# Optimization experiments

Hardware: AMD Instinct MI355X
Metric: run time of the kernel (lower is better)

## Reference

```python
import jax, jax.numpy as jnp
import numpy as np

EPS = 0.1        # SinkhornDistance eps (hard-coded in SGE.__init__)
MAX_ITER = 10    # SinkhornDistance max_iter
THRESH = 0.1     # early-exit threshold in SinkhornDistance.forward
N_POINTS = 32
SPACE_DIM = 16   # emb_dim // n_points = 512 // 32


def _sinkhorn_cost(x, y):
    """Regularized OT cost between point clouds x, y: [B, P, D] -> [B]."""
    # C[b,i,j] = sum_d |x[b,i,d] - y[b,j,d]|^2
    C = jnp.sum(jnp.square(jnp.abs(x[:, :, None, :] - y[:, None, :, :])), axis=-1)
    B, P1 = x.shape[0], x.shape[1]
    P2 = y.shape[1]
    mu = jnp.full((B, P1), 1.0 / P1, dtype=x.dtype)
    nu = jnp.full((B, P2), 1.0 / P2, dtype=x.dtype)

    def M(u, v):
        # (-C + u_i + v_j) / eps
        return (-C + u[:, :, None] + v[:, None, :]) / EPS

    def step(carry, _):
        u, v, done = carry
        u_new = EPS * (jnp.log(mu + 1e-8) - jax.nn.logsumexp(M(u, v), axis=-1)) + u
        v_new = EPS * (jnp.log(nu + 1e-8)
                       - jax.nn.logsumexp(M(u_new, v).swapaxes(-2, -1), axis=-1)) + v
        err = jnp.mean(jnp.sum(jnp.abs(u_new - u), axis=-1))
        u2 = jnp.where(done, u, u_new)
        v2 = jnp.where(done, v, v_new)
        done2 = done | (err < THRESH)  # torch breaks AFTER applying the update
        return (u2, v2, done2), None

    init = (jnp.zeros_like(mu), jnp.zeros_like(nu), jnp.array(False))
    (u, v, _), _ = jax.lax.scan(step, init, None, length=MAX_ITER)
    pi = jnp.exp(M(u, v))
    return jnp.sum(pi * C, axis=(-2, -1))  # [B]


def setup_inputs() -> dict:
    key = jax.random.key(0)
    k1, k2, k3, k4 = jax.random.split(key, 4)
    n_nodes, feat, emb, n_edges = 10000, 256, 512, 4096
    x = jax.random.normal(k1, (n_nodes, feat), dtype=jnp.float32)
    W = jax.random.normal(k2, (feat, emb), dtype=jnp.float32) / np.float32(np.sqrt(feat))
    edges_pos = jax.random.randint(k3, (2, n_edges), 0, n_nodes)
    edges_neg = jax.random.randint(k4, (2, n_edges), 0, n_nodes)
    return {"x": x, "W": W, "edges_pos": edges_pos, "edges_neg": edges_neg}


def reference(x, W, edges_pos, edges_neg):
    z = x @ W  # encoder: linear projection [n_nodes, emb_dim]

    def score_pairs(nx, ny):
        a = z[nx].reshape(-1, N_POINTS, SPACE_DIM)
        b = z[ny].reshape(-1, N_POINTS, SPACE_DIM)
        return -_sinkhorn_cost(a, b)

    pos_energy = score_pairs(edges_pos[0], edges_pos[1])
    neg_energy = score_pairs(edges_neg[0], edges_neg[1])
    loss = jnp.mean(pos_energy ** 2 + jnp.exp(neg_energy))
    return loss
```

## Files before the change

kernel.cpp:

```cpp
#include <hip/hip_runtime.h>
#include <hip/hip_bf16.h>
#include <math.h>

#define N_POINTS 32
#define SPACE_DIM 16
#define EMB 512
#define THRESH 0.1f
#define MAX_ITER 10
#define KDIM 256

#define NEG10LOG2E -14.42695040888963f
#define EPS_LN2     0.0693147180559945f
#define LOGMU2     -4.99999953834f

typedef _Float16 half8 __attribute__((ext_vector_type(8)));
typedef _Float16 half4 __attribute__((ext_vector_type(4)));
typedef float floatx4 __attribute__((ext_vector_type(4)));

#define BSTRIDE 264

__global__ __launch_bounds__(256) void gemm_fused(
    const float* __restrict__ X, const float* __restrict__ W,
    float* __restrict__ Z, int M, int K, int N)
{
    (void)K;

    __shared__ _Float16 Bs[64][BSTRIDE];

    int t = threadIdx.x;
    int n0 = blockIdx.y * 64;

    int wave = t >> 6;
    int lane = t & 63;
    int quad = lane >> 4;
    int l16 = lane & 15;

    int mrow = blockIdx.x * 64 + wave * 16 + l16;
    int msafe = mrow < M ? mrow : M - 1;
    const float4* xp = (const float4*)(X + (size_t)msafe * KDIM);

    float4 xr[16];
    #pragma unroll
    for (int kk = 0; kk < 8; ++kk) {
        xr[2 * kk]     = xp[kk * 8 + quad * 2];
        xr[2 * kk + 1] = xp[kk * 8 + quad * 2 + 1];
    }

    #pragma unroll
    for (int s = 0; s < 4; ++s) {
        int u = s * 256 + t;
        int nb = u & 15;
        int kb = u >> 4;
        float4 r0v = *(const float4*)&W[(size_t)(kb * 4 + 0) * N + n0 + nb * 4];
        float4 r1v = *(const float4*)&W[(size_t)(kb * 4 + 1) * N + n0 + nb * 4];
        float4 r2v = *(const float4*)&W[(size_t)(kb * 4 + 2) * N + n0 + nb * 4];
        float4 r3v = *(const float4*)&W[(size_t)(kb * 4 + 3) * N + n0 + nb * 4];
        float c0[4] = {r0v.x, r0v.y, r0v.z, r0v.w};
        float c1[4] = {r1v.x, r1v.y, r1v.z, r1v.w};
        float c2[4] = {r2v.x, r2v.y, r2v.z, r2v.w};
        float c3[4] = {r3v.x, r3v.y, r3v.z, r3v.w};
        #pragma unroll
        for (int c = 0; c < 4; ++c) {
            half4 h = {(_Float16)c0[c], (_Float16)c1[c],
                       (_Float16)c2[c], (_Float16)c3[c]};
            *(half4*)&Bs[nb * 4 + c][kb * 4] = h;
        }
    }
    __syncthreads();

    floatx4 acc[4] = {{0.f,0.f,0.f,0.f},{0.f,0.f,0.f,0.f},
                      {0.f,0.f,0.f,0.f},{0.f,0.f,0.f,0.f}};

    #pragma unroll
    for (int kk = 0; kk < 8; ++kk) {
        float4 lo = xr[2 * kk];
        float4 hi = xr[2 * kk + 1];
        half8 a = {(_Float16)lo.x, (_Float16)lo.y, (_Float16)lo.z, (_Float16)lo.w,
                   (_Float16)hi.x, (_Float16)hi.y, (_Float16)hi.z, (_Float16)hi.w};
        #pragma unroll
        for (int ct = 0; ct < 4; ++ct) {
            half8 b = *(const half8*)&Bs[ct * 16 + l16][kk * 32 + quad * 8];
            acc[ct] = __builtin_amdgcn_mfma_f32_16x16x32_f16(a, b, acc[ct], 0, 0, 0);
        }
    }

    int rbase = blockIdx.x * 64 + wave * 16 + quad * 4;
    #pragma unroll
    for (int ct = 0; ct < 4; ++ct) {
        int col = n0 + ct * 16 + l16;
        #pragma unroll
        for (int r = 0; r < 4; ++r) {
            int row = rbase + r;
            if (row < M) Z[(size_t)row * N + col] = acc[ct][r];
        }
    }
}

#define WPB 4

__global__ __launch_bounds__(256, 4) void sinkhorn_fused(
    const float* __restrict__ Z,
    const int* __restrict__ ep, const int* __restrict__ en,
    int nE,
    float* __restrict__ cost_all,
    float* __restrict__ err_part)
{
    __shared__ float shm[WPB][32 * 36];
    __shared__ float uvs[WPB][64];

    int tid = threadIdx.x;
    int wv = tid >> 6;
    int t = tid & 63;
    int b = blockIdx.x * WPB + wv;

    int side = (b >= nE) ? 1 : 0;
    int e = b - side * nE;
    const int* edges = side ? en : ep;
    int nx = edges[e];
    int ny = edges[e + nE];

    int c = t & 31;
    int h = t >> 5;
    int r0 = h * 16;

    float* sb  = shm[wv];
    float* csh = shm[wv];
    float* Ul  = uvs[wv];
    float* Vl  = uvs[wv] + 32;

    {
        const float4* zb4 = (const float4*)(Z + (size_t)ny * EMB);
        float4 q0 = zb4[t * 2];
        float4 q1 = zb4[t * 2 + 1];
        float* dst = sb + (t >> 1) * 20 + (t & 1) * 8;
        ((float4*)dst)[0] = q0;
        ((float4*)dst)[1] = q1;
    }
    float areg[16];
    {
        const float4* za4 = (const float4*)(Z + (size_t)nx * EMB + c * SPACE_DIM);
        float4 a0 = za4[0], a1 = za4[1], a2 = za4[2], a3 = za4[3];
        areg[0]=a0.x; areg[1]=a0.y; areg[2]=a0.z; areg[3]=a0.w;
        areg[4]=a1.x; areg[5]=a1.y; areg[6]=a1.z; areg[7]=a1.w;
        areg[8]=a2.x; areg[9]=a2.y; areg[10]=a2.z; areg[11]=a2.w;
        areg[12]=a3.x; areg[13]=a3.y; areg[14]=a3.z; areg[15]=a3.w;
    }

    float Crow[16];
    #pragma unroll
    for (int jj = 0; jj < 16; ++jj) {
        const float* bp = sb + (r0 + jj) * 20;
        float s = 0.f;
        #pragma unroll
        for (int d = 0; d < SPACE_DIM; ++d) {
            float diff = areg[d] - bp[d];
            s = fmaf(diff, diff, s);
        }
        Crow[jj] = s * NEG10LOG2E;
    }
    #pragma unroll
    for (int g = 0; g < 4; ++g) {
        *(float4*)&csh[c * 36 + r0 + g * 4] =
            make_float4(Crow[g*4+0], Crow[g*4+1], Crow[g*4+2], Crow[g*4+3]);
    }
    float Ccol[16];
    #pragma unroll
    for (int ii = 0; ii < 16; ++ii)
        Ccol[ii] = csh[(r0 + ii) * 36 + c];

    Vl[c] = 0.f;
    float U = 0.f;
    float ccp[MAX_ITER];
    float dup[MAX_ITER];

    #pragma unroll
    for (int it = 0; it < MAX_ITER; ++it) {
        float w[16];
        {
            const float4* vp = (const float4*)(Vl + r0);
            float4 v0 = vp[0], v1 = vp[1], v2 = vp[2], v3 = vp[3];
            float vv[16] = {v0.x,v0.y,v0.z,v0.w, v1.x,v1.y,v1.z,v1.w,
                            v2.x,v2.y,v2.z,v2.w, v3.x,v3.y,v3.z,v3.w};
            #pragma unroll
            for (int jj = 0; jj < 16; ++jj) w[jj] = Crow[jj] + vv[jj];
        }
        float m8[8];
        #pragma unroll
        for (int k = 0; k < 8; ++k) m8[k] = fmaxf(w[k], w[k + 8]);
        float m4a = fmaxf(m8[0], m8[4]), m4b = fmaxf(m8[1], m8[5]);
        float m4c = fmaxf(m8[2], m8[6]), m4d = fmaxf(m8[3], m8[7]);
        float mx = fmaxf(fmaxf(m4a, m4b), fmaxf(m4c, m4d));
        mx = fmaxf(mx, __shfl_xor(mx, 32));

        float ex[16];
        #pragma unroll
        for (int jj = 0; jj < 16; ++jj) ex[jj] = __builtin_amdgcn_exp2f(w[jj] - mx);
        float s8[8], p8[8];
        #pragma unroll
        for (int k = 0; k < 8; ++k) {
            s8[k] = ex[k] + ex[k + 8];
            p8[k] = fmaf(ex[k], Crow[k], ex[k + 8] * Crow[k + 8]);
        }
        float sm = ((s8[0]+s8[4]) + (s8[1]+s8[5])) + ((s8[2]+s8[6]) + (s8[3]+s8[7]));
        float pc = ((p8[0]+p8[4]) + (p8[1]+p8[5])) + ((p8[2]+p8[6]) + (p8[3]+p8[7]));
        sm += __shfl_xor(sm, 32);

        if (it > 0) ccp[it - 1] = __builtin_amdgcn_exp2f(U + mx) * pc;

        float Un = LOGMU2 - (mx + __builtin_amdgcn_logf(sm));
        dup[it] = fabsf(Un - U);
        U = Un;
        Ul[c] = U;

        float wc[16];
        {
            const float4* up = (const float4*)(Ul + r0);
            float4 u0 = up[0], u1 = up[1], u2 = up[2], u3 = up[3];
            float uu[16] = {u0.x,u0.y,u0.z,u0.w, u1.x,u1.y,u1.z,u1.w,
                            u2.x,u2.y,u2.z,u2.w, u3.x,u3.y,u3.z,u3.w};
            #pragma unroll
            for (int ii = 0; ii < 16; ++ii) wc[ii] = Ccol[ii] + uu[ii];
        }
        float n8[8];
        #pragma unroll
        for (int k = 0; k < 8; ++k) n8[k] = fmaxf(wc[k], wc[k + 8]);
        float n4a = fmaxf(n8[0], n8[4]), n4b = fmaxf(n8[1], n8[5]);
        float n4c = fmaxf(n8[2], n8[6]), n4d = fmaxf(n8[3], n8[7]);
        float mx2 = fmaxf(fmaxf(n4a, n4b), fmaxf(n4c, n4d));
        mx2 = fmaxf(mx2, __shfl_xor(mx2, 32));

        float e2[16];
        #pragma unroll
        for (int ii = 0; ii < 16; ++ii) e2[ii] = __builtin_amdgcn_exp2f(wc[ii] - mx2);
        float t8[8];
        #pragma unroll
        for (int k = 0; k < 8; ++k) t8[k] = e2[k] + e2[k + 8];
        float sm2 = ((t8[0]+t8[4]) + (t8[1]+t8[5])) + ((t8[2]+t8[6]) + (t8[3]+t8[7]));
        sm2 += __shfl_xor(sm2, 32);
        float Vn = LOGMU2 - (mx2 + __builtin_amdgcn_logf(sm2));
        Vl[c] = Vn;
    }

    {
        const float4* vp = (const float4*)(Vl + r0);
        float4 v0 = vp[0], v1 = vp[1], v2 = vp[2], v3 = vp[3];
        float vv[16] = {v0.x,v0.y,v0.z,v0.w, v1.x,v1.y,v1.z,v1.w,
                        v2.x,v2.y,v2.z,v2.w, v3.x,v3.y,v3.z,v3.w};
        float cc = 0.f;
        #pragma unroll
        for (int jj = 0; jj < 16; ++jj)
            cc = fmaf(__builtin_amdgcn_exp2f(U + Crow[jj] + vv[jj]), Crow[jj], cc);
        ccp[MAX_ITER - 1] = cc;
    }

    #pragma unroll
    for (int m = 1; m < 32; m <<= 1) {
        #pragma unroll
        for (int k = 0; k < MAX_ITER; ++k) {
            dup[k] += __shfl_xor(dup[k], m);
            ccp[k] += __shfl_xor(ccp[k], m);
        }
    }
    #pragma unroll
    for (int k = 0; k < MAX_ITER; ++k) ccp[k] += __shfl_xor(ccp[k], 32);

    if (t == 0) {
        #pragma unroll
        for (int k = 0; k < MAX_ITER; ++k)
            cost_all[(size_t)k * (2 * nE) + b] = -EPS_LN2 * ccp[k];
        #pragma unroll
        for (int k = 0; k < MAX_ITER; ++k) uvs[wv][k] = dup[k];
    }
    __syncthreads();

    if (tid < MAX_ITER) {
        float s4 = uvs[0][tid] + uvs[1][tid] + uvs[2][tid] + uvs[3][tid];
        err_part[(size_t)tid * gridDim.x + blockIdx.x] = EPS_LN2 * s4;
    }
}

__global__ __launch_bounds__(256) void finalize(
    const float* __restrict__ err_part,
    const float* __restrict__ cost_all,
    float* __restrict__ out, int nE, int nB)
{
    __shared__ float em_s[2 * MAX_ITER];
    __shared__ float red[4];

    int tid = threadIdx.x;
    int wv = tid >> 6;
    int t = tid & 63;

    for (int r = wv; r < MAX_ITER; r += 4) {
        const float4* p4 = (const float4*)(err_part + (size_t)r * nB);
        float4 v0 = p4[t       ], v1 = p4[t +  64], v2 = p4[t + 128], v3 = p4[t + 192];
        float4 v4 = p4[t + 256], v5 = p4[t + 320], v6 = p4[t + 384], v7 = p4[t + 448];
        float ps = ((v0.x+v0.y)+(v0.z+v0.w)) + ((v1.x+v1.y)+(v1.z+v1.w))
                 + ((v2.x+v2.y)+(v2.z+v2.w)) + ((v3.x+v3.y)+(v3.z+v3.w));
        float ns = ((v4.x+v4.y)+(v4.z+v4.w)) + ((v5.x+v5.y)+(v5.z+v5.w))
                 + ((v6.x+v6.y)+(v6.z+v6.w)) + ((v7.x+v7.y)+(v7.z+v7.w));
        #pragma unroll
        for (int m = 1; m < 64; m <<= 1) {
            ps += __shfl_xor(ps, m);
            ns += __shfl_xor(ns, m);
        }
        if (t == 0) {
            em_s[r] = ps / (float)nE;
            em_s[MAX_ITER + r] = ns / (float)nE;
        }
    }
    __syncthreads();

    int Tp = MAX_ITER, Tn = MAX_ITER;
    for (int i = 0; i < MAX_ITER; ++i)
        if (em_s[i] < THRESH) { Tp = i + 1; break; }
    for (int i = 0; i < MAX_ITER; ++i)
        if (em_s[MAX_ITER + i] < THRESH) { Tn = i + 1; break; }

    const float4* cp4 = (const float4*)(cost_all + (size_t)(Tp - 1) * (2 * nE));
    const float4* cn4 = (const float4*)(cost_all + (size_t)(Tn - 1) * (2 * nE) + nE);
    float4 p0 = cp4[tid      ], p1 = cp4[tid + 256],
           p2 = cp4[tid + 512], p3 = cp4[tid + 768];
    float4 n0 = cn4[tid      ], n1 = cn4[tid + 256],
           n2 = cn4[tid + 512], n3 = cn4[tid + 768];
    float aP = 0.f;
    aP = fmaf(p0.x,p0.x,aP); aP = fmaf(p0.y,p0.y,aP);
    aP = fmaf(p0.z,p0.z,aP); aP = fmaf(p0.w,p0.w,aP);
    aP = fmaf(p1.x,p1.x,aP); aP = fmaf(p1.y,p1.y,aP);
    aP = fmaf(p1.z,p1.z,aP); aP = fmaf(p1.w,p1.w,aP);
    aP = fmaf(p2.x,p2.x,aP); aP = fmaf(p2.y,p2.y,aP);
    aP = fmaf(p2.z,p2.z,aP); aP = fmaf(p2.w,p2.w,aP);
    aP = fmaf(p3.x,p3.x,aP); aP = fmaf(p3.y,p3.y,aP);
    aP = fmaf(p3.z,p3.z,aP); aP = fmaf(p3.w,p3.w,aP);
    float aN = 0.f;
    aN += expf(-n0.x) + expf(-n0.y) + expf(-n0.z) + expf(-n0.w);
    aN += expf(-n1.x) + expf(-n1.y) + expf(-n1.z) + expf(-n1.w);
    aN += expf(-n2.x) + expf(-n2.y) + expf(-n2.z) + expf(-n2.w);
    aN += expf(-n3.x) + expf(-n3.y) + expf(-n3.z) + expf(-n3.w);
    float acc = aP + aN;
    #pragma unroll
    for (int m = 1; m < 64; m <<= 1) acc += __shfl_xor(acc, m);
    if (t == 0) red[wv] = acc;
    __syncthreads();
    if (tid == 0)
        out[0] = ((red[0] + red[1]) + (red[2] + red[3])) / (float)nE;
}

extern "C" void kernel_launch(void* const* d_in, const int* in_sizes, int n_in,
                              void* d_out, int out_size, void* d_ws, size_t ws_size,
                              hipStream_t stream)
{
    const float* X = (const float*)d_in[0];
    const float* W = (const float*)d_in[1];
    const int* ep = (const int*)d_in[2];
    const int* en = (const int*)d_in[3];
    float* out = (float*)d_out;

    int K = in_sizes[1] / EMB;
    int M = in_sizes[0] / K;
    int nE = in_sizes[2] / 2;

    float* ws = (float*)d_ws;
    float* Z = ws;
    float* cost_all = Z + (size_t)M * EMB;
    float* err_part = cost_all + (size_t)MAX_ITER * 2 * nE;

    dim3 gg((M + 63) / 64, EMB / 64);
    gemm_fused<<<gg, 256, 0, stream>>>(X, W, Z, M, K, EMB);

    int nblk = (2 * nE) / WPB;
    sinkhorn_fused<<<nblk, 64 * WPB, 0, stream>>>(Z, ep, en, nE,
                                                  cost_all, err_part);

    finalize<<<1, 256, 0, stream>>>(err_part, cost_all, out, nE, nblk);
}
```

Baseline: 136.5 us.

## Widen GEMM blocks to 256 columns with double-buffered W staging

Each GEMM block now covers 256 output columns in four 64-column chunks instead of one, so the X rows are loaded and converted to fp16 once and reused across the chunks. The W tile for the next chunk is staged into a second shared-memory buffer while the current chunk runs its MFMAs, overlapping global loads with compute. The grid shrinks from 8 to 2 column blocks, which cuts redundant X traffic but lowers parallelism (about 314 blocks) and doubles LDS use per block, which can reduce occupancy.

```diff
diff --git a/kernel.cpp b/kernel.cpp
--- a/kernel.cpp
+++ b/kernel.cpp
@@ -25,73 +25,81 @@
 {
     (void)K;
 
-    __shared__ _Float16 Bs[64][BSTRIDE];
+    __shared__ _Float16 Bs[2][64][BSTRIDE];
 
     int t = threadIdx.x;
-    int n0 = blockIdx.y * 64;
-
     int wave = t >> 6;
     int lane = t & 63;
     int quad = lane >> 4;
     int l16 = lane & 15;
+    int n_base = blockIdx.y * 256;
 
     int mrow = blockIdx.x * 64 + wave * 16 + l16;
     int msafe = mrow < M ? mrow : M - 1;
     const float4* xp = (const float4*)(X + (size_t)msafe * KDIM);
 
-    float4 xr[16];
+    half8 ah[8];
     #pragma unroll
     for (int kk = 0; kk < 8; ++kk) {
-        xr[2 * kk]     = xp[kk * 8 + quad * 2];
-        xr[2 * kk + 1] = xp[kk * 8 + quad * 2 + 1];
-    }
-
-    #pragma unroll
-    for (int s = 0; s < 4; ++s) {
-        int u = s * 256 + t;
-        int nb = u & 15;
-        int kb = u >> 4;
-        float4 r0v = *(const float4*)&W[(size_t)(kb * 4 + 0) * N + n0 + nb * 4];
-        float4 r1v = *(const float4*)&W[(size_t)(kb * 4 + 1) * N + n0 + nb * 4];
-        float4 r2v = *(const float4*)&W[(size_t)(kb * 4 + 2) * N + n0 + nb * 4];
-        float4 r3v = *(const float4*)&W[(size_t)(kb * 4 + 3) * N + n0 + nb * 4];
-        float c0[4] = {r0v.x, r0v.y, r0v.z, r0v.w};
-        float c1[4] = {r1v.x, r1v.y, r1v.z, r1v.w};
-        float c2[4] = {r2v.x, r2v.y, r2v.z, r2v.w};
-        float c3[4] = {r3v.x, r3v.y, r3v.z, r3v.w};
-        #pragma unroll
-        for (int c = 0; c < 4; ++c) {
-            half4 h = {(_Float16)c0[c], (_Float16)c1[c],
-                       (_Float16)c2[c], (_Float16)c3[c]};
-            *(half4*)&Bs[nb * 4 + c][kb * 4] = h;
-        }
-    }
-    __syncthreads();
-
-    floatx4 acc[4] = {{0.f,0.f,0.f,0.f},{0.f,0.f,0.f,0.f},
-                      {0.f,0.f,0.f,0.f},{0.f,0.f,0.f,0.f}};
-
-    #pragma unroll
-    for (int kk = 0; kk < 8; ++kk) {
-        float4 lo = xr[2 * kk];
-        float4 hi = xr[2 * kk + 1];
-        half8 a = {(_Float16)lo.x, (_Float16)lo.y, (_Float16)lo.z, (_Float16)lo.w,
-                   (_Float16)hi.x, (_Float16)hi.y, (_Float16)hi.z, (_Float16)hi.w};
+        float4 lo = xp[kk * 8 + quad * 2];
+        float4 hi = xp[kk * 8 + quad * 2 + 1];
+        ah[kk] = (half8){(_Float16)lo.x, (_Float16)lo.y, (_Float16)lo.z, (_Float16)lo.w,
+                         (_Float16)hi.x, (_Float16)hi.y, (_Float16)hi.z, (_Float16)hi.w};
+    }
+
+    auto stage = [&](int buf, int ct2) {
+        int n0 = n_base + ct2 * 64;
+        #pragma unroll
+        for (int s = 0; s < 4; ++s) {
+            int u = s * 256 + t;
+            int nb = u & 15;
+            int kb = u >> 4;
+            float4 r0v = *(const float4*)&W[(size_t)(kb * 4 + 0) * N + n0 + nb * 4];
+            float4 r1v = *(const float4*)&W[(size_t)(kb * 4 + 1) * N + n0 + nb * 4];
+            float4 r2v = *(const float4*)&W[(size_t)(kb * 4 + 2) * N + n0 + nb * 4];
+            float4 r3v = *(const float4*)&W[(size_t)(kb * 4 + 3) * N + n0 + nb * 4];
+            float c0[4] = {r0v.x, r0v.y, r0v.z, r0v.w};
+            float c1[4] = {r1v.x, r1v.y, r1v.z, r1v.w};
+            float c2[4] = {r2v.x, r2v.y, r2v.z, r2v.w};
+            float c3[4] = {r3v.x, r3v.y, r3v.z, r3v.w};
+            #pragma unroll
+            for (int c = 0; c < 4; ++c) {
+                half4 h = {(_Float16)c0[c], (_Float16)c1[c],
+                           (_Float16)c2[c], (_Float16)c3[c]};
+                *(half4*)&Bs[buf][nb * 4 + c][kb * 4] = h;
+            }
+        }
+    };
+
+    stage(0, 0);
+
+    int rbase = blockIdx.x * 64 + wave * 16 + quad * 4;
+
+    #pragma unroll
+    for (int ct2 = 0; ct2 < 4; ++ct2) {
+        __syncthreads();
+        if (ct2 < 3) stage((ct2 + 1) & 1, ct2 + 1);
+
+        int cur = ct2 & 1;
+        floatx4 acc[4] = {{0.f,0.f,0.f,0.f},{0.f,0.f,0.f,0.f},
+                          {0.f,0.f,0.f,0.f},{0.f,0.f,0.f,0.f}};
+        #pragma unroll
+        for (int kk = 0; kk < 8; ++kk) {
+            #pragma unroll
+            for (int ct = 0; ct < 4; ++ct) {
+                half8 b = *(const half8*)&Bs[cur][ct * 16 + l16][kk * 32 + quad * 8];
+                acc[ct] = __builtin_amdgcn_mfma_f32_16x16x32_f16(ah[kk], b, acc[ct], 0, 0, 0);
+            }
+        }
+
         #pragma unroll
         for (int ct = 0; ct < 4; ++ct) {
-            half8 b = *(const half8*)&Bs[ct * 16 + l16][kk * 32 + quad * 8];
-            acc[ct] = __builtin_amdgcn_mfma_f32_16x16x32_f16(a, b, acc[ct], 0, 0, 0);
-        }
-    }
-
-    int rbase = blockIdx.x * 64 + wave * 16 + quad * 4;
-    #pragma unroll
-    for (int ct = 0; ct < 4; ++ct) {
-        int col = n0 + ct * 16 + l16;
-        #pragma unroll
-        for (int r = 0; r < 4; ++r) {
-            int row = rbase + r;
-            if (row < M) Z[(size_t)row * N + col] = acc[ct][r];
+            int col = n_base + ct2 * 64 + ct * 16 + l16;
+            #pragma unroll
+            for (int r = 0; r < 4; ++r) {
+                int row = rbase + r;
+                if (row < M) Z[(size_t)row * N + col] = acc[ct][r];
+            }
         }
     }
 }
@@ -365,7 +373,7 @@
     float* cost_all = Z + (size_t)M * EMB;
     float* err_part = cost_all + (size_t)MAX_ITER * 2 * nE;
 
-    dim3 gg((M + 63) / 64, EMB / 64);
+    dim3 gg((M + 63) / 64, 2);
     gemm_fused<<<gg, 256, 0, stream>>>(X, W, Z, M, K, EMB);
 
     int nblk = (2 * nE) / WPB;
```

Result: no change. 134.1 us (median of 2 runs) (-1.8%).
